# Kernel tuning notes

Hardware: AMD Instinct MI355X
Metric: run time of the kernel (lower is better)

Reference implementation:

```python
import jax, jax.numpy as jnp
import numpy as np
from jax import lax

T, H, I, E = 1024, 2048, 1024, 16
G, TOPK_GROUP, TOP_K = 4, 2, 4
ROUTED_SCALE = 2.5
W_SCALE = 0.02  # keep activations in a sane range


def setup_inputs() -> dict:
    key = jax.random.key(0)
    ks = jax.random.split(key, 7)
    return {
        "hidden_states": jax.random.normal(ks[0], (T, H), jnp.float32),
        "gate_w": jax.random.normal(ks[1], (E, H), jnp.float32) * W_SCALE,
        "e_bias": jax.random.normal(ks[2], (E,), jnp.float32),
        "w_gate_up": jax.random.normal(ks[3], (E, 2 * I, H), jnp.float32) * W_SCALE,
        "w_down": jax.random.normal(ks[4], (E, H, I), jnp.float32) * W_SCALE,
        "shared_w_gate_up": jax.random.normal(ks[5], (2 * I, H), jnp.float32) * W_SCALE,
        "shared_w_down": jax.random.normal(ks[6], (H, I), jnp.float32) * W_SCALE,
    }


def _grouped_topk(scores, e_bias):
    # scores: sigmoid router scores [T, E]
    scores_b = scores + e_bias[None, :]
    # group score = sum of top-2 biased scores within each group (bias branch)
    group_scores = jnp.sum(lax.top_k(scores_b.reshape(-1, G, E // G), 2)[0], axis=-1)  # [T, G]
    _, group_idx = lax.top_k(group_scores, TOPK_GROUP)  # [T, topk_group]
    group_mask = jnp.any(jax.nn.one_hot(group_idx, G, dtype=jnp.bool_), axis=1)  # [T, G]
    score_mask = jnp.repeat(group_mask, E // G, axis=-1)  # [T, E]
    tmp = jnp.where(score_mask, scores_b, 0.0)
    _, topk_ids = lax.top_k(tmp, TOP_K)  # [T, K]
    topk_w = jnp.take_along_axis(scores, topk_ids, axis=1)  # weights from UNbiased scores
    topk_w = topk_w / jnp.sum(topk_w, axis=-1, keepdims=True)  # renormalize
    return topk_w, topk_ids


def _silu_and_mul(gu):
    g, u = jnp.split(gu, 2, axis=-1)
    return jax.nn.silu(g) * u


def reference(hidden_states, gate_w, e_bias, w_gate_up, w_down,
              shared_w_gate_up, shared_w_down):
    x = hidden_states  # [T, H]
    # shared expert MLP
    shared = _silu_and_mul(x @ shared_w_gate_up.T) @ shared_w_down.T  # [T, H]
    # router
    logits = x @ gate_w.T                      # [T, E]
    scores = jax.nn.sigmoid(logits)
    topk_w, topk_ids = _grouped_topk(scores, e_bias)
    # dense combine weights [T, E] (zero for unselected experts)
    combine = jnp.zeros((T, E), x.dtype).at[jnp.arange(T)[:, None], topk_ids].add(topk_w)
    # routed experts: SwiGLU per expert, combined with routing weights
    gu = jnp.einsum('th,eih->tei', x, w_gate_up)        # [T, E, 2I]
    a = _silu_and_mul(gu)                               # [T, E, I]
    routed = jnp.einsum('tei,ehi,te->th', a, w_down, combine)  # [T, H]
    return routed * ROUTED_SCALE + shared
```

## Files before the change

kernel.cpp:

```cpp
#include <hip/hip_runtime.h>
#include <math.h>

typedef __bf16 bf16;
typedef bf16 bf16x4 __attribute__((ext_vector_type(4)));
typedef bf16 bf16x8 __attribute__((ext_vector_type(8)));
typedef float f32x4 __attribute__((ext_vector_type(4)));

#define T_TOK   1024
#define H_DIM   2048
#define I_DIM   1024
#define NPAIR_R 4096
#define NPAIR   5120
#define BK      32
#define LDSS    40
#define ABUF    10240
#define BUFSZ   20480
#define SMEM_SZ 40960

__device__ inline bf16x8 cvt8(const float4 a, const float4 b) {
  bf16x8 r;
  r[0] = (bf16)a.x; r[1] = (bf16)a.y; r[2] = (bf16)a.z; r[3] = (bf16)a.w;
  r[4] = (bf16)b.x; r[5] = (bf16)b.y; r[6] = (bf16)b.z; r[7] = (bf16)b.w;
  return r;
}

__global__ __launch_bounds__(256) void router_kernel(
    const float* __restrict__ x, const float* __restrict__ gate_w,
    const float* __restrict__ e_bias,
    int* __restrict__ topk_ids, float* __restrict__ topk_w,
    int* __restrict__ counts)
{
  int t = blockIdx.x;
  int tid = threadIdx.x;
  float acc[16];
#pragma unroll
  for (int e = 0; e < 16; ++e) acc[e] = 0.f;
  const float* xr = x + (size_t)t * H_DIM;
  for (int h = tid; h < H_DIM; h += 256) {
    float xv = xr[h];
#pragma unroll
    for (int e = 0; e < 16; ++e) acc[e] += xv * gate_w[e * H_DIM + h];
  }
#pragma unroll
  for (int e = 0; e < 16; ++e) {
#pragma unroll
    for (int off = 32; off >= 1; off >>= 1)
      acc[e] += __shfl_down(acc[e], off, 64);
  }
  __shared__ float red[4][16];
  int lane = tid & 63, wave = tid >> 6;
  if (lane == 0) {
#pragma unroll
    for (int e = 0; e < 16; ++e) red[wave][e] = acc[e];
  }
  __syncthreads();
  if (tid == 0) {
    float scores[16], sb[16];
    for (int e = 0; e < 16; ++e) {
      float l = red[0][e] + red[1][e] + red[2][e] + red[3][e];
      float s = 1.f / (1.f + expf(-l));
      scores[e] = s;
      sb[e] = s + e_bias[e];
    }
    float gs[4];
    for (int g = 0; g < 4; ++g) {
      float b1 = -1e30f, b2 = -1e30f;
      for (int j = 0; j < 4; ++j) {
        float v = sb[g * 4 + j];
        if (v > b1) { b2 = b1; b1 = v; }
        else if (v > b2) b2 = v;
      }
      gs[g] = b1 + b2;
    }
    int g1 = 0; float bv = gs[0];
    for (int g = 1; g < 4; ++g) if (gs[g] > bv) { bv = gs[g]; g1 = g; }
    int g2 = -1; float bv2 = -1e30f;
    for (int g = 0; g < 4; ++g) if (g != g1 && gs[g] > bv2) { bv2 = gs[g]; g2 = g; }
    float tmp[16];
    for (int e = 0; e < 16; ++e) {
      int grp = e >> 2;
      tmp[e] = (grp == g1 || grp == g2) ? sb[e] : 0.0f;
    }
    bool used[16] = {false};
    int ids[4]; float wv[4]; float wsum = 0.f;
    for (int k = 0; k < 4; ++k) {
      int bi = 0; float bvv = -1e30f;
      for (int i = 0; i < 16; ++i)
        if (!used[i] && tmp[i] > bvv) { bvv = tmp[i]; bi = i; }
      used[bi] = true;
      ids[k] = bi; wv[k] = scores[bi]; wsum += scores[bi];
    }
    float inv = 1.f / wsum;
    for (int k = 0; k < 4; ++k) {
      topk_ids[t * 4 + k] = ids[k];
      topk_w[t * 4 + k] = wv[k] * inv;
      atomicAdd(&counts[ids[k]], 1);
    }
  }
}

__global__ void offsets_kernel(const int* __restrict__ counts, int* __restrict__ off)
{
  if (threadIdx.x == 0 && blockIdx.x == 0) {
    int s = 0;
    for (int e = 0; e < 16; ++e) { off[e] = s; s += counts[e]; }
    off[16] = s;
  }
}

__global__ __launch_bounds__(256) void scatter_kernel(
    const int* __restrict__ topk_ids, const float* __restrict__ topk_w,
    const int* __restrict__ off, int* __restrict__ cursor,
    int* __restrict__ pair_token, float* __restrict__ pair_scale,
    int* __restrict__ inv_pair)
{
  int i = blockIdx.x * 256 + threadIdx.x;
  if (i < NPAIR_R) {
    int e = topk_ids[i];
    float w = topk_w[i];
    int pos = atomicAdd(&cursor[e], 1);
    int idx = off[e] + pos;
    int t = i >> 2;
    pair_token[idx] = t;
    pair_scale[idx] = 2.5f * w;
    inv_pair[t * 5 + (i & 3)] = idx;
  } else if (i < NPAIR) {
    int t = i - NPAIR_R;
    pair_token[i] = t;
    pair_scale[i] = 1.0f;
    inv_pair[t * 5 + 4] = i;
  }
}

__global__ __launch_bounds__(256) void gateup_silu_kernel(
    const float* __restrict__ x, const float* __restrict__ w_gu,
    const float* __restrict__ s_wgu,
    const int* __restrict__ off, const int* __restrict__ pair_token,
    bf16* __restrict__ a_buf)
{
  const int nt = blockIdx.x;
  const int mt = blockIdx.y;
  const int e  = blockIdx.z;
  const int poff = (e < 16) ? off[e]     : NPAIR_R;
  const int pend = (e < 16) ? off[e + 1] : NPAIR;
  const int cnt  = pend - poff;
  if (mt * 128 >= cnt) return;
  const float* __restrict__ B = (e < 16) ? (w_gu + (size_t)e * 2 * I_DIM * H_DIM) : s_wgu;

  __shared__ char smem[SMEM_SZ];

  const int tid = threadIdx.x;
  const int lane = tid & 63, wave = tid >> 6;
  const int wm = wave >> 1, wn = wave & 1;
  const int srow = tid >> 1;
  const int scol = (tid & 1) * 16;
  const int l15 = lane & 15;
  const int kq = (lane >> 4) * 8;

  int rloc = mt * 128 + srow;
  int p_eff = poff + (rloc < cnt ? rloc : cnt - 1);
  const float* __restrict__ Arow = x + (size_t)pair_token[p_eff] * H_DIM + scol;
  int brow_g = nt * 64 + (srow < 64 ? srow : 960 + srow);
  const float* __restrict__ Brow = B + (size_t)brow_g * H_DIM + scol;

  f32x4 acc[4][4];
#pragma unroll
  for (int mi = 0; mi < 4; ++mi)
#pragma unroll
    for (int ni = 0; ni < 4; ++ni) { acc[mi][ni][0]=0.f; acc[mi][ni][1]=0.f; acc[mi][ni][2]=0.f; acc[mi][ni][3]=0.f; }

  float4 ar[4], br[4];
#pragma unroll
  for (int i = 0; i < 4; ++i) {
    ar[i] = *(const float4*)(Arow + 4 * i);
    br[i] = *(const float4*)(Brow + 4 * i);
  }
  {
    bf16* As = (bf16*)(smem);
    bf16* Bs = (bf16*)(smem + ABUF);
    *(bf16x8*)(As + srow * LDSS + scol)     = cvt8(ar[0], ar[1]);
    *(bf16x8*)(As + srow * LDSS + scol + 8) = cvt8(ar[2], ar[3]);
    *(bf16x8*)(Bs + srow * LDSS + scol)     = cvt8(br[0], br[1]);
    *(bf16x8*)(Bs + srow * LDSS + scol + 8) = cvt8(br[2], br[3]);
  }
  __syncthreads();
  int cur = 0;
  for (int k0 = BK; ; k0 += BK) {
    const bool more = (k0 < H_DIM);
    if (more) {
#pragma unroll
      for (int i = 0; i < 4; ++i) {
        ar[i] = *(const float4*)(Arow + k0 + 4 * i);
        br[i] = *(const float4*)(Brow + k0 + 4 * i);
      }
    }
    {
      const bf16* As = (const bf16*)(smem + cur * BUFSZ);
      const bf16* Bs = (const bf16*)(smem + cur * BUFSZ + ABUF);
      bf16x8 af[4], bfv[4];
#pragma unroll
      for (int mi = 0; mi < 4; ++mi)
        af[mi] = *(const bf16x8*)(As + (wm * 64 + mi * 16 + l15) * LDSS + kq);
#pragma unroll
      for (int ni = 0; ni < 4; ++ni)
        bfv[ni] = *(const bf16x8*)(Bs + (wn * 64 + ni * 16 + l15) * LDSS + kq);
#pragma unroll
      for (int mi = 0; mi < 4; ++mi)
#pragma unroll
        for (int ni = 0; ni < 4; ++ni)
          acc[mi][ni] = __builtin_amdgcn_mfma_f32_16x16x32_bf16(af[mi], bfv[ni], acc[mi][ni], 0, 0, 0);
    }
    if (more) {
      bf16* As = (bf16*)(smem + (cur ^ 1) * BUFSZ);
      bf16* Bs = (bf16*)(smem + (cur ^ 1) * BUFSZ + ABUF);
      *(bf16x8*)(As + srow * LDSS + scol)     = cvt8(ar[0], ar[1]);
      *(bf16x8*)(As + srow * LDSS + scol + 8) = cvt8(ar[2], ar[3]);
      *(bf16x8*)(Bs + srow * LDSS + scol)     = cvt8(br[0], br[1]);
      *(bf16x8*)(Bs + srow * LDSS + scol + 8) = cvt8(br[2], br[3]);
    }
    __syncthreads();
    cur ^= 1;
    if (!more) break;
  }

  float* u_lds = (float*)smem;
  if (wn == 1) {
#pragma unroll
    for (int mi = 0; mi < 4; ++mi)
#pragma unroll
      for (int reg = 0; reg < 4; ++reg) {
        int r = wm * 64 + mi * 16 + (lane >> 4) * 4 + reg;
#pragma unroll
        for (int ni = 0; ni < 4; ++ni)
          u_lds[r * 65 + ni * 16 + l15] = acc[mi][ni][reg];
      }
  }
  __syncthreads();
  if (wn == 0) {
#pragma unroll
    for (int mi = 0; mi < 4; ++mi)
#pragma unroll
      for (int reg = 0; reg < 4; ++reg) {
        int r = wm * 64 + mi * 16 + (lane >> 4) * 4 + reg;
        int rl = mt * 128 + r;
        if (rl < cnt) {
          bf16* orow = a_buf + (size_t)(poff + rl) * I_DIM + nt * 64 + l15;
#pragma unroll
          for (int ni = 0; ni < 4; ++ni) {
            float g = acc[mi][ni][reg];
            float u = u_lds[r * 65 + ni * 16 + l15];
            float s = g / (1.f + __expf(-g));
            orow[ni * 16] = (bf16)(s * u);
          }
        }
      }
  }
}

__global__ __launch_bounds__(256) void down_kernel(
    const bf16* __restrict__ a_buf, const float* __restrict__ w_dn,
    const float* __restrict__ s_wdn,
    const int* __restrict__ off, const float* __restrict__ pair_scale,
    bf16* __restrict__ dpart)
{
  const int nt = blockIdx.x;
  const int mt = blockIdx.y;
  const int e  = blockIdx.z;
  const int poff = (e < 16) ? off[e]     : NPAIR_R;
  const int pend = (e < 16) ? off[e + 1] : NPAIR;
  const int cnt  = pend - poff;
  if (mt * 128 >= cnt) return;
  const float* __restrict__ B = (e < 16) ? (w_dn + (size_t)e * H_DIM * I_DIM) : s_wdn;

  __shared__ char smem[SMEM_SZ];

  const int tid = threadIdx.x;
  const int lane = tid & 63, wave = tid >> 6;
  const int wm = wave >> 1, wn = wave & 1;
  const int srow = tid >> 1;
  const int scol = (tid & 1) * 16;
  const int l15 = lane & 15;
  const int kq = (lane >> 4) * 8;

  int rloc = mt * 128 + srow;
  int r_eff = poff + (rloc < cnt ? rloc : cnt - 1);
  const bf16* __restrict__ Arow = a_buf + (size_t)r_eff * I_DIM + scol;
  const float* __restrict__ Brow = B + (size_t)(nt * 128 + srow) * I_DIM + scol;

  f32x4 acc[4][4];
#pragma unroll
  for (int mi = 0; mi < 4; ++mi)
#pragma unroll
    for (int ni = 0; ni < 4; ++ni) { acc[mi][ni][0]=0.f; acc[mi][ni][1]=0.f; acc[mi][ni][2]=0.f; acc[mi][ni][3]=0.f; }

  bf16x8 a0, a1; float4 br[4];
  a0 = *(const bf16x8*)(Arow);
  a1 = *(const bf16x8*)(Arow + 8);
#pragma unroll
  for (int i = 0; i < 4; ++i) br[i] = *(const float4*)(Brow + 4 * i);
  {
    bf16* As = (bf16*)(smem);
    bf16* Bs = (bf16*)(smem + ABUF);
    *(bf16x8*)(As + srow * LDSS + scol)     = a0;
    *(bf16x8*)(As + srow * LDSS + scol + 8) = a1;
    *(bf16x8*)(Bs + srow * LDSS + scol)     = cvt8(br[0], br[1]);
    *(bf16x8*)(Bs + srow * LDSS + scol + 8) = cvt8(br[2], br[3]);
  }
  __syncthreads();
  int cur = 0;
  for (int k0 = BK; ; k0 += BK) {
    const bool more = (k0 < I_DIM);
    if (more) {
      a0 = *(const bf16x8*)(Arow + k0);
      a1 = *(const bf16x8*)(Arow + k0 + 8);
#pragma unroll
      for (int i = 0; i < 4; ++i) br[i] = *(const float4*)(Brow + k0 + 4 * i);
    }
    {
      const bf16* As = (const bf16*)(smem + cur * BUFSZ);
      const bf16* Bs = (const bf16*)(smem + cur * BUFSZ + ABUF);
      bf16x8 af[4], bfv[4];
#pragma unroll
      for (int mi = 0; mi < 4; ++mi)
        af[mi] = *(const bf16x8*)(As + (wm * 64 + mi * 16 + l15) * LDSS + kq);
#pragma unroll
      for (int ni = 0; ni < 4; ++ni)
        bfv[ni] = *(const bf16x8*)(Bs + (wn * 64 + ni * 16 + l15) * LDSS + kq);
#pragma unroll
      for (int mi = 0; mi < 4; ++mi)
#pragma unroll
        for (int ni = 0; ni < 4; ++ni)
          acc[mi][ni] = __builtin_amdgcn_mfma_f32_16x16x32_bf16(af[mi], bfv[ni], acc[mi][ni], 0, 0, 0);
    }
    if (more) {
      bf16* As = (bf16*)(smem + (cur ^ 1) * BUFSZ);
      bf16* Bs = (bf16*)(smem + (cur ^ 1) * BUFSZ + ABUF);
      *(bf16x8*)(As + srow * LDSS + scol)     = a0;
      *(bf16x8*)(As + srow * LDSS + scol + 8) = a1;
      *(bf16x8*)(Bs + srow * LDSS + scol)     = cvt8(br[0], br[1]);
      *(bf16x8*)(Bs + srow * LDSS + scol + 8) = cvt8(br[2], br[3]);
    }
    __syncthreads();
    cur ^= 1;
    if (!more) break;
  }

  const int colb = nt * 128 + wn * 64;
#pragma unroll
  for (int mi = 0; mi < 4; ++mi) {
#pragma unroll
    for (int reg = 0; reg < 4; ++reg) {
      int r = wm * 64 + mi * 16 + (lane >> 4) * 4 + reg;
      int rl = mt * 128 + r;
      if (rl < cnt) {
        int p = poff + rl;
        float sc = pair_scale[p];
        bf16* orow = dpart + (size_t)p * H_DIM + colb + l15;
#pragma unroll
        for (int ni = 0; ni < 4; ++ni)
          orow[ni * 16] = (bf16)(acc[mi][ni][reg] * sc);
      }
    }
  }
}

__global__ __launch_bounds__(256) void combine_kernel(
    const bf16* __restrict__ dpart, const int* __restrict__ inv_pair,
    float* __restrict__ out)
{
  int i = (blockIdx.x * 256 + threadIdx.x) * 4;
  int t = i >> 11;
  int h = i & 2047;
  const int* iv = inv_pair + t * 5;
  float4 s = {0.f, 0.f, 0.f, 0.f};
#pragma unroll
  for (int j = 0; j < 5; ++j) {
    bf16x4 d = *(const bf16x4*)(dpart + (size_t)iv[j] * H_DIM + h);
    s.x += (float)d[0]; s.y += (float)d[1]; s.z += (float)d[2]; s.w += (float)d[3];
  }
  *(float4*)(out + i) = s;
}

extern "C" void kernel_launch(void* const* d_in, const int* in_sizes, int n_in,
                              void* d_out, int out_size, void* d_ws, size_t ws_size,
                              hipStream_t stream)
{
  const float* x     = (const float*)d_in[0];
  const float* gatew = (const float*)d_in[1];
  const float* ebias = (const float*)d_in[2];
  const float* w_gu  = (const float*)d_in[3];
  const float* w_dn  = (const float*)d_in[4];
  const float* s_wgu = (const float*)d_in[5];
  const float* s_wdn = (const float*)d_in[6];
  float* out = (float*)d_out;

  char* ws = (char*)d_ws;
  int*   off        = (int*)(ws + 0);
  int*   counts     = (int*)(ws + 128);
  int*   cursor     = (int*)(ws + 192);
  int*   topk_ids   = (int*)(ws + 256);
  float* topk_w     = (float*)(ws + 16640);
  int*   pair_token = (int*)(ws + 33024);
  float* pair_scale = (float*)(ws + 53504);
  int*   inv_pair   = (int*)(ws + 73984);
  bf16*  a_buf      = (bf16*)(ws + 94464);
  bf16*  dpart      = (bf16*)(ws + 10580224);

  hipMemsetAsync(ws + 128, 0, 128, stream);

  router_kernel<<<T_TOK, 256, 0, stream>>>(x, gatew, ebias, topk_ids, topk_w, counts);
  offsets_kernel<<<1, 64, 0, stream>>>(counts, off);
  scatter_kernel<<<NPAIR / 256, 256, 0, stream>>>(topk_ids, topk_w, off, cursor,
                                                  pair_token, pair_scale, inv_pair);
  dim3 g1(16, 8, 17);
  gateup_silu_kernel<<<g1, 256, 0, stream>>>(x, w_gu, s_wgu, off, pair_token, a_buf);
  dim3 g2(16, 8, 17);
  down_kernel<<<g2, 256, 0, stream>>>(a_buf, w_dn, s_wdn, off, pair_scale, dpart);
  combine_kernel<<<(T_TOK * H_DIM) / (256 * 4), 256, 0, stream>>>(dpart, inv_pair, out);
}
```

Before: 688.2 us.

## Stage GEMM tiles via direct global-to-LDS loads with XOR swizzle and smaller M tiles

Both expert GEMM kernels now copy fp32 (and bf16) tiles straight from global memory into LDS with global_load_lds, using an XOR-swizzled layout, and convert to bf16 only when reading fragments from LDS. The register-staged double buffer is dropped, so each K step loads, syncs, then computes. M tiles shrink from 128 to 64 rows for more blocks and less padding waste on uneven expert counts. The shared expert is moved to blockIdx.z 0 so it is scheduled first. The gate/up kernel keeps gate and up accumulators in the same thread, which removes the LDS exchange in the SiLU epilogue. In exchange, LDS traffic doubles because tiles are stored as fp32, and with no prefetch the loads are no longer overlapped with the MFMAs.

```diff
diff --git a/kernel.cpp b/kernel.cpp
--- a/kernel.cpp
+++ b/kernel.cpp
@@ -11,13 +11,15 @@
 #define I_DIM   1024
 #define NPAIR_R 4096
 #define NPAIR   5120
-#define BK      32
-#define LDSS    40
-#define ABUF    10240
-#define BUFSZ   20480
-#define SMEM_SZ 40960
-
-__device__ inline bf16x8 cvt8(const float4 a, const float4 b) {
+
+typedef __attribute__((address_space(3))) void lds_void;
+typedef const __attribute__((address_space(1))) void glob_void;
+
+__device__ __forceinline__ void gl16(const void* g, void* l) {
+  __builtin_amdgcn_global_load_lds((glob_void*)g, (lds_void*)l, 16, 0, 0);
+}
+
+__device__ __forceinline__ bf16x8 cvt8(const float4 a, const float4 b) {
   bf16x8 r;
   r[0] = (bf16)a.x; r[1] = (bf16)a.y; r[2] = (bf16)a.z; r[3] = (bf16)a.w;
   r[4] = (bf16)b.x; r[5] = (bf16)b.y; r[6] = (bf16)b.z; r[7] = (bf16)b.w;
@@ -140,121 +142,110 @@
 {
   const int nt = blockIdx.x;
   const int mt = blockIdx.y;
-  const int e  = blockIdx.z;
+  const int ez = blockIdx.z;
+  const int e  = (ez == 0) ? 16 : ez - 1;
   const int poff = (e < 16) ? off[e]     : NPAIR_R;
   const int pend = (e < 16) ? off[e + 1] : NPAIR;
   const int cnt  = pend - poff;
-  if (mt * 128 >= cnt) return;
-  const float* __restrict__ B = (e < 16) ? (w_gu + (size_t)e * 2 * I_DIM * H_DIM) : s_wgu;
-
-  __shared__ char smem[SMEM_SZ];
+  if (mt * 64 >= cnt) return;
+  const float* __restrict__ B = (e < 16) ? (w_gu + (size_t)e * (2 * I_DIM) * H_DIM) : s_wgu;
+
+  __shared__ __attribute__((aligned(16))) char smem[24576];
 
   const int tid = threadIdx.x;
   const int lane = tid & 63, wave = tid >> 6;
   const int wm = wave >> 1, wn = wave & 1;
-  const int srow = tid >> 1;
-  const int scol = (tid & 1) * 16;
-  const int l15 = lane & 15;
-  const int kq = (lane >> 4) * 8;
-
-  int rloc = mt * 128 + srow;
-  int p_eff = poff + (rloc < cnt ? rloc : cnt - 1);
-  const float* __restrict__ Arow = x + (size_t)pair_token[p_eff] * H_DIM + scol;
-  int brow_g = nt * 64 + (srow < 64 ? srow : 960 + srow);
-  const float* __restrict__ Brow = B + (size_t)brow_g * H_DIM + scol;
-
-  f32x4 acc[4][4];
-#pragma unroll
-  for (int mi = 0; mi < 4; ++mi)
-#pragma unroll
-    for (int ni = 0; ni < 4; ++ni) { acc[mi][ni][0]=0.f; acc[mi][ni][1]=0.f; acc[mi][ni][2]=0.f; acc[mi][ni][3]=0.f; }
-
-  float4 ar[4], br[4];
-#pragma unroll
-  for (int i = 0; i < 4; ++i) {
-    ar[i] = *(const float4*)(Arow + 4 * i);
-    br[i] = *(const float4*)(Brow + 4 * i);
-  }
-  {
-    bf16* As = (bf16*)(smem);
-    bf16* Bs = (bf16*)(smem + ABUF);
-    *(bf16x8*)(As + srow * LDSS + scol)     = cvt8(ar[0], ar[1]);
-    *(bf16x8*)(As + srow * LDSS + scol + 8) = cvt8(ar[2], ar[3]);
-    *(bf16x8*)(Bs + srow * LDSS + scol)     = cvt8(br[0], br[1]);
-    *(bf16x8*)(Bs + srow * LDSS + scol + 8) = cvt8(br[2], br[3]);
-  }
-  __syncthreads();
-  int cur = 0;
-  for (int k0 = BK; ; k0 += BK) {
-    const bool more = (k0 < H_DIM);
-    if (more) {
-#pragma unroll
-      for (int i = 0; i < 4; ++i) {
-        ar[i] = *(const float4*)(Arow + k0 + 4 * i);
-        br[i] = *(const float4*)(Brow + k0 + 4 * i);
-      }
-    }
-    {
-      const bf16* As = (const bf16*)(smem + cur * BUFSZ);
-      const bf16* Bs = (const bf16*)(smem + cur * BUFSZ + ABUF);
-      bf16x8 af[4], bfv[4];
-#pragma unroll
-      for (int mi = 0; mi < 4; ++mi)
-        af[mi] = *(const bf16x8*)(As + (wm * 64 + mi * 16 + l15) * LDSS + kq);
-#pragma unroll
-      for (int ni = 0; ni < 4; ++ni)
-        bfv[ni] = *(const bf16x8*)(Bs + (wn * 64 + ni * 16 + l15) * LDSS + kq);
-#pragma unroll
-      for (int mi = 0; mi < 4; ++mi)
-#pragma unroll
-        for (int ni = 0; ni < 4; ++ni)
-          acc[mi][ni] = __builtin_amdgcn_mfma_f32_16x16x32_bf16(af[mi], bfv[ni], acc[mi][ni], 0, 0, 0);
-    }
-    if (more) {
-      bf16* As = (bf16*)(smem + (cur ^ 1) * BUFSZ);
-      bf16* Bs = (bf16*)(smem + (cur ^ 1) * BUFSZ + ABUF);
-      *(bf16x8*)(As + srow * LDSS + scol)     = cvt8(ar[0], ar[1]);
-      *(bf16x8*)(As + srow * LDSS + scol + 8) = cvt8(ar[2], ar[3]);
-      *(bf16x8*)(Bs + srow * LDSS + scol)     = cvt8(br[0], br[1]);
-      *(bf16x8*)(Bs + srow * LDSS + scol + 8) = cvt8(br[2], br[3]);
-    }
+  const int l15 = lane & 15, q = lane >> 4;
+
+  const float* a_src[2];
+#pragma unroll
+  for (int i = 0; i < 2; ++i) {
+    int flat = wave * 2048 + i * 1024 + lane * 16;
+    int r = flat >> 7;
+    int c = ((flat >> 4) & 7) ^ (r & 7);
+    int rg = mt * 64 + r; if (rg >= cnt) rg = cnt - 1;
+    a_src[i] = x + (size_t)pair_token[poff + rg] * H_DIM + c * 4;
+  }
+  const float* b_src[4];
+#pragma unroll
+  for (int j = 0; j < 4; ++j) {
+    int flat = wave * 4096 + j * 1024 + lane * 16;
+    int r = flat >> 7;
+    int c = ((flat >> 4) & 7) ^ (r & 7);
+    int brow = nt * 64 + ((r < 64) ? r : (960 + r));
+    b_src[j] = B + (size_t)brow * H_DIM + c * 4;
+  }
+  char* aw = smem + wave * 2048;
+  char* bw = smem + 8192 + wave * 4096;
+
+  f32x4 accg[2][2], accu[2][2];
+#pragma unroll
+  for (int mi = 0; mi < 2; ++mi)
+#pragma unroll
+    for (int ni = 0; ni < 2; ++ni) {
+      accg[mi][ni][0]=0.f; accg[mi][ni][1]=0.f; accg[mi][ni][2]=0.f; accg[mi][ni][3]=0.f;
+      accu[mi][ni][0]=0.f; accu[mi][ni][1]=0.f; accu[mi][ni][2]=0.f; accu[mi][ni][3]=0.f;
+    }
+
+  for (int k0 = 0; k0 < H_DIM; k0 += 32) {
+    gl16(a_src[0] + k0, aw);
+    gl16(a_src[1] + k0, aw + 1024);
+#pragma unroll
+    for (int j = 0; j < 4; ++j) gl16(b_src[j] + k0, bw + j * 1024);
     __syncthreads();
-    cur ^= 1;
-    if (!more) break;
-  }
-
-  float* u_lds = (float*)smem;
-  if (wn == 1) {
-#pragma unroll
-    for (int mi = 0; mi < 4; ++mi)
-#pragma unroll
-      for (int reg = 0; reg < 4; ++reg) {
-        int r = wm * 64 + mi * 16 + (lane >> 4) * 4 + reg;
-#pragma unroll
-        for (int ni = 0; ni < 4; ++ni)
-          u_lds[r * 65 + ni * 16 + l15] = acc[mi][ni][reg];
-      }
-  }
-  __syncthreads();
-  if (wn == 0) {
-#pragma unroll
-    for (int mi = 0; mi < 4; ++mi)
-#pragma unroll
-      for (int reg = 0; reg < 4; ++reg) {
-        int r = wm * 64 + mi * 16 + (lane >> 4) * 4 + reg;
-        int rl = mt * 128 + r;
-        if (rl < cnt) {
-          bf16* orow = a_buf + (size_t)(poff + rl) * I_DIM + nt * 64 + l15;
-#pragma unroll
-          for (int ni = 0; ni < 4; ++ni) {
-            float g = acc[mi][ni][reg];
-            float u = u_lds[r * 65 + ni * 16 + l15];
-            float s = g / (1.f + __expf(-g));
-            orow[ni * 16] = (bf16)(s * u);
-          }
+
+    bf16x8 af[2], bg[2], bu[2];
+#pragma unroll
+    for (int mi = 0; mi < 2; ++mi) {
+      int r = wm * 32 + mi * 16 + l15;
+      int c0 = (2 * q) ^ (r & 7), c1 = (2 * q + 1) ^ (r & 7);
+      float4 v0 = *(const float4*)(smem + r * 128 + c0 * 16);
+      float4 v1 = *(const float4*)(smem + r * 128 + c1 * 16);
+      af[mi] = cvt8(v0, v1);
+    }
+#pragma unroll
+    for (int ni = 0; ni < 2; ++ni) {
+      int rg2 = wn * 32 + ni * 16 + l15;
+      {
+        int c0 = (2 * q) ^ (rg2 & 7), c1 = (2 * q + 1) ^ (rg2 & 7);
+        float4 v0 = *(const float4*)(smem + 8192 + rg2 * 128 + c0 * 16);
+        float4 v1 = *(const float4*)(smem + 8192 + rg2 * 128 + c1 * 16);
+        bg[ni] = cvt8(v0, v1);
+      }
+      int ru = 64 + rg2;
+      {
+        int c0 = (2 * q) ^ (ru & 7), c1 = (2 * q + 1) ^ (ru & 7);
+        float4 v0 = *(const float4*)(smem + 8192 + ru * 128 + c0 * 16);
+        float4 v1 = *(const float4*)(smem + 8192 + ru * 128 + c1 * 16);
+        bu[ni] = cvt8(v0, v1);
+      }
+    }
+#pragma unroll
+    for (int mi = 0; mi < 2; ++mi)
+#pragma unroll
+      for (int ni = 0; ni < 2; ++ni) {
+        accg[mi][ni] = __builtin_amdgcn_mfma_f32_16x16x32_bf16(af[mi], bg[ni], accg[mi][ni], 0, 0, 0);
+        accu[mi][ni] = __builtin_amdgcn_mfma_f32_16x16x32_bf16(af[mi], bu[ni], accu[mi][ni], 0, 0, 0);
+      }
+    __syncthreads();
+  }
+
+#pragma unroll
+  for (int mi = 0; mi < 2; ++mi)
+#pragma unroll
+    for (int reg = 0; reg < 4; ++reg) {
+      int rr = wm * 32 + mi * 16 + q * 4 + reg;
+      int rg = mt * 64 + rr;
+      if (rg < cnt) {
+        bf16* orow = a_buf + (size_t)(poff + rg) * I_DIM + nt * 64 + wn * 32 + l15;
+#pragma unroll
+        for (int ni = 0; ni < 2; ++ni) {
+          float g = accg[mi][ni][reg];
+          float u = accu[mi][ni][reg];
+          orow[ni * 16] = (bf16)(g / (1.f + __expf(-g)) * u);
         }
       }
-  }
+    }
 }
 
 __global__ __launch_bounds__(256) void down_kernel(
@@ -265,103 +256,90 @@
 {
   const int nt = blockIdx.x;
   const int mt = blockIdx.y;
-  const int e  = blockIdx.z;
+  const int ez = blockIdx.z;
+  const int e  = (ez == 0) ? 16 : ez - 1;
   const int poff = (e < 16) ? off[e]     : NPAIR_R;
   const int pend = (e < 16) ? off[e + 1] : NPAIR;
   const int cnt  = pend - poff;
-  if (mt * 128 >= cnt) return;
+  if (mt * 64 >= cnt) return;
   const float* __restrict__ B = (e < 16) ? (w_dn + (size_t)e * H_DIM * I_DIM) : s_wdn;
 
-  __shared__ char smem[SMEM_SZ];
+  __shared__ __attribute__((aligned(16))) char smem[20480];
 
   const int tid = threadIdx.x;
   const int lane = tid & 63, wave = tid >> 6;
   const int wm = wave >> 1, wn = wave & 1;
-  const int srow = tid >> 1;
-  const int scol = (tid & 1) * 16;
-  const int l15 = lane & 15;
-  const int kq = (lane >> 4) * 8;
-
-  int rloc = mt * 128 + srow;
-  int r_eff = poff + (rloc < cnt ? rloc : cnt - 1);
-  const bf16* __restrict__ Arow = a_buf + (size_t)r_eff * I_DIM + scol;
-  const float* __restrict__ Brow = B + (size_t)(nt * 128 + srow) * I_DIM + scol;
-
-  f32x4 acc[4][4];
-#pragma unroll
-  for (int mi = 0; mi < 4; ++mi)
+  const int l15 = lane & 15, q = lane >> 4;
+
+  const bf16* a_src;
+  {
+    int flat = wave * 1024 + lane * 16;
+    int r = flat >> 6;
+    int c = ((flat >> 4) & 3) ^ ((r >> 1) & 3);
+    int rg = mt * 64 + r; if (rg >= cnt) rg = cnt - 1;
+    a_src = a_buf + (size_t)(poff + rg) * I_DIM + c * 8;
+  }
+  const float* b_src[4];
+#pragma unroll
+  for (int j = 0; j < 4; ++j) {
+    int flat = wave * 4096 + j * 1024 + lane * 16;
+    int r = flat >> 7;
+    int c = ((flat >> 4) & 7) ^ (r & 7);
+    b_src[j] = B + (size_t)(nt * 128 + r) * I_DIM + c * 4;
+  }
+  char* aw = smem + wave * 1024;
+  char* bw = smem + 4096 + wave * 4096;
+
+  f32x4 acc[2][4];
+#pragma unroll
+  for (int mi = 0; mi < 2; ++mi)
 #pragma unroll
     for (int ni = 0; ni < 4; ++ni) { acc[mi][ni][0]=0.f; acc[mi][ni][1]=0.f; acc[mi][ni][2]=0.f; acc[mi][ni][3]=0.f; }
 
-  bf16x8 a0, a1; float4 br[4];
-  a0 = *(const bf16x8*)(Arow);
-  a1 = *(const bf16x8*)(Arow + 8);
-#pragma unroll
-  for (int i = 0; i < 4; ++i) br[i] = *(const float4*)(Brow + 4 * i);
-  {
-    bf16* As = (bf16*)(smem);
-    bf16* Bs = (bf16*)(smem + ABUF);
-    *(bf16x8*)(As + srow * LDSS + scol)     = a0;
-    *(bf16x8*)(As + srow * LDSS + scol + 8) = a1;
-    *(bf16x8*)(Bs + srow * LDSS + scol)     = cvt8(br[0], br[1]);
-    *(bf16x8*)(Bs + srow * LDSS + scol + 8) = cvt8(br[2], br[3]);
-  }
-  __syncthreads();
-  int cur = 0;
-  for (int k0 = BK; ; k0 += BK) {
-    const bool more = (k0 < I_DIM);
-    if (more) {
-      a0 = *(const bf16x8*)(Arow + k0);
-      a1 = *(const bf16x8*)(Arow + k0 + 8);
-#pragma unroll
-      for (int i = 0; i < 4; ++i) br[i] = *(const float4*)(Brow + k0 + 4 * i);
-    }
-    {
-      const bf16* As = (const bf16*)(smem + cur * BUFSZ);
-      const bf16* Bs = (const bf16*)(smem + cur * BUFSZ + ABUF);
-      bf16x8 af[4], bfv[4];
-#pragma unroll
-      for (int mi = 0; mi < 4; ++mi)
-        af[mi] = *(const bf16x8*)(As + (wm * 64 + mi * 16 + l15) * LDSS + kq);
+  for (int k0 = 0; k0 < I_DIM; k0 += 32) {
+    gl16(a_src + k0, aw);
+#pragma unroll
+    for (int j = 0; j < 4; ++j) gl16(b_src[j] + k0, bw + j * 1024);
+    __syncthreads();
+
+    bf16x8 af[2], bfv[4];
+#pragma unroll
+    for (int mi = 0; mi < 2; ++mi) {
+      int r = wm * 32 + mi * 16 + l15;
+      int c = q ^ ((r >> 1) & 3);
+      af[mi] = *(const bf16x8*)(smem + r * 64 + c * 16);
+    }
+#pragma unroll
+    for (int ni = 0; ni < 4; ++ni) {
+      int r = wn * 64 + ni * 16 + l15;
+      int c0 = (2 * q) ^ (r & 7), c1 = (2 * q + 1) ^ (r & 7);
+      float4 v0 = *(const float4*)(smem + 4096 + r * 128 + c0 * 16);
+      float4 v1 = *(const float4*)(smem + 4096 + r * 128 + c1 * 16);
+      bfv[ni] = cvt8(v0, v1);
+    }
+#pragma unroll
+    for (int mi = 0; mi < 2; ++mi)
 #pragma unroll
       for (int ni = 0; ni < 4; ++ni)
-        bfv[ni] = *(const bf16x8*)(Bs + (wn * 64 + ni * 16 + l15) * LDSS + kq);
-#pragma unroll
-      for (int mi = 0; mi < 4; ++mi)
-#pragma unroll
-        for (int ni = 0; ni < 4; ++ni)
-          acc[mi][ni] = __builtin_amdgcn_mfma_f32_16x16x32_bf16(af[mi], bfv[ni], acc[mi][ni], 0, 0, 0);
-    }
-    if (more) {
-      bf16* As = (bf16*)(smem + (cur ^ 1) * BUFSZ);
-      bf16* Bs = (bf16*)(smem + (cur ^ 1) * BUFSZ + ABUF);
-      *(bf16x8*)(As + srow * LDSS + scol)     = a0;
-      *(bf16x8*)(As + srow * LDSS + scol + 8) = a1;
-      *(bf16x8*)(Bs + srow * LDSS + scol)     = cvt8(br[0], br[1]);
-      *(bf16x8*)(Bs + srow * LDSS + scol + 8) = cvt8(br[2], br[3]);
-    }
+        acc[mi][ni] = __builtin_amdgcn_mfma_f32_16x16x32_bf16(af[mi], bfv[ni], acc[mi][ni], 0, 0, 0);
     __syncthreads();
-    cur ^= 1;
-    if (!more) break;
-  }
-
-  const int colb = nt * 128 + wn * 64;
-#pragma unroll
-  for (int mi = 0; mi < 4; ++mi) {
+  }
+
+#pragma unroll
+  for (int mi = 0; mi < 2; ++mi)
 #pragma unroll
     for (int reg = 0; reg < 4; ++reg) {
-      int r = wm * 64 + mi * 16 + (lane >> 4) * 4 + reg;
-      int rl = mt * 128 + r;
-      if (rl < cnt) {
-        int p = poff + rl;
+      int rr = wm * 32 + mi * 16 + q * 4 + reg;
+      int rg = mt * 64 + rr;
+      if (rg < cnt) {
+        int p = poff + rg;
         float sc = pair_scale[p];
-        bf16* orow = dpart + (size_t)p * H_DIM + colb + l15;
+        bf16* orow = dpart + (size_t)p * H_DIM + nt * 128 + wn * 64 + l15;
 #pragma unroll
         for (int ni = 0; ni < 4; ++ni)
           orow[ni * 16] = (bf16)(acc[mi][ni][reg] * sc);
       }
     }
-  }
 }
 
 __global__ __launch_bounds__(256) void combine_kernel(
@@ -396,8 +374,6 @@
 
   char* ws = (char*)d_ws;
   int*   off        = (int*)(ws + 0);
-  int*   counts     = (int*)(ws + 128);
-  int*   cursor     = (int*)(ws + 192);
   int*   topk_ids   = (int*)(ws + 256);
   float* topk_w     = (float*)(ws + 16640);
   int*   pair_token = (int*)(ws + 33024);
@@ -405,6 +381,8 @@
   int*   inv_pair   = (int*)(ws + 73984);
   bf16*  a_buf      = (bf16*)(ws + 94464);
   bf16*  dpart      = (bf16*)(ws + 10580224);
+  int*   counts     = (int*)(ws + 128);
+  int*   cursor     = (int*)(ws + 192);
 
   hipMemsetAsync(ws + 128, 0, 128, stream);
 
@@ -412,9 +390,9 @@
   offsets_kernel<<<1, 64, 0, stream>>>(counts, off);
   scatter_kernel<<<NPAIR / 256, 256, 0, stream>>>(topk_ids, topk_w, off, cursor,
                                                   pair_token, pair_scale, inv_pair);
-  dim3 g1(16, 8, 17);
+  dim3 g1(16, 16, 17);
   gateup_silu_kernel<<<g1, 256, 0, stream>>>(x, w_gu, s_wgu, off, pair_token, a_buf);
-  dim3 g2(16, 8, 17);
+  dim3 g2(16, 16, 17);
   down_kernel<<<g2, 256, 0, stream>>>(a_buf, w_dn, s_wdn, off, pair_scale, dpart);
   combine_kernel<<<(T_TOK * H_DIM) / (256 * 4), 256, 0, stream>>>(dpart, inv_pair, out);
 }
```

Measured after the change: 679.2 us. No clear change (-1.3%).
